# Kernel optimization log

Hardware: AMD Instinct MI355X
Metric: run time of the kernel (lower is better)

## Reference

```python
import jax, jax.numpy as jnp
import numpy as np

B, H, L, E, M = 16, 8, 4096, 64, 64


def setup_inputs() -> dict:
    key = jax.random.key(0)
    k1, k2, k3 = jax.random.split(key, 3)
    x = jax.random.normal(k1, (B, H, L, E), dtype=jnp.float32)
    # nn.Parameter(torch.randn(E, E, M, 2) / sqrt(E))
    weights = jax.random.normal(k2, (E, E, M, 2), dtype=jnp.float32) / np.float32(np.sqrt(E))
    # torch.randperm(L//2)[:M].sort()[0] -> sorted unique mode indices in [0, L//2)
    index = jnp.sort(jax.random.permutation(k3, L // 2)[:M]).astype(jnp.int32)
    return {"x": x, "weights": weights, "index": index}


def reference(x, weights, index):
    Bx, Hx, Lx, Ex = x.shape
    xt = jnp.swapaxes(x, -1, -2)                      # [B,H,E,L]
    x_ft = jnp.fft.rfft(xt, axis=-1)                  # [B,H,E,L//2+1] complex64
    w_c = jax.lax.complex(weights[..., 0], weights[..., 1])  # [E,E,M] complex
    sel = x_ft[..., index]                            # gather K modes: [B,H,E,M]
    out_sel = jnp.einsum('bhei,eoi->bhoi', sel, w_c)  # per-mode complex matmul
    out_ft = jnp.zeros_like(x_ft).at[..., index].set(out_sel)  # scatter back
    out = jnp.fft.irfft(out_ft, n=Lx, axis=-1)        # [B,H,E,L] real
    return jnp.swapaxes(out, -1, -2)                  # [B,H,L,E]
```

## Files before the change

### kernel.cpp

```cpp
#include <hip/hip_runtime.h>

using half8 = __attribute__((ext_vector_type(8))) _Float16;
using f32x4 = __attribute__((ext_vector_type(4))) float;
using u16x4 = __attribute__((ext_vector_type(4))) unsigned short;

#define Lc 4096
#define Ec 64
#define Mc 64
#define BHc 128

#define TWO_PI_OVER_L 1.5339807878856412e-3f

__global__ __launch_bounds__(256) void twid_k(const int* __restrict__ idx,
                                              _Float16* __restrict__ Tt,
                                              _Float16* __restrict__ UL) {
    int id = blockIdx.x * 256 + threadIdx.x;
    {
        int l = id >> 7, m2 = id & 127, m = m2 & 63;
        int k = idx[m];
        int ph = (k * l) & (Lc - 1);
        float ang = (float)ph * TWO_PI_OVER_L;
        UL[id] = (_Float16)((m2 >= 64) ? __sinf(ang) : __cosf(ang));
    }
    {
        int m2 = id >> 12, l = id & 4095, m = m2 & 63;
        int k = idx[m];
        int ph = (k * l) & (Lc - 1);
        float ang = (float)ph * TWO_PI_OVER_L;
        Tt[id] = (_Float16)((m2 >= 64) ? -__sinf(ang) : __cosf(ang));
    }
}

#define LOADT(SET, S) do{                                                     \
    const float* g0_ = xp + (size_t)((S) * 64 + 2 * lp) * Ec;                 \
    const float* g1_ = xp + (size_t)((S) * 64 + 2 * lp + 32) * Ec;            \
    ra[SET][0] = *(const float4*)g0_;  rb[SET][0] = *(const float4*)(g0_ + Ec);\
    ra[SET][1] = *(const float4*)g1_;  rb[SET][1] = *(const float4*)(g1_ + Ec);\
}while(0)

#define PACKT(SET, BUF) do{                                                   \
    _Pragma("unroll")                                                         \
    for (int i_ = 0; i_ < 2; ++i_) {                                          \
        const float* pa_ = (const float*)&ra[SET][i_];                        \
        const float* pb_ = (const float*)&rb[SET][i_];                        \
        unsigned int pk_[4];                                                  \
        _Pragma("unroll")                                                     \
        for (int j_ = 0; j_ < 4; ++j_) {                                      \
            unsigned short ua_ = __builtin_bit_cast(unsigned short, (_Float16)pa_[j_]); \
            unsigned short ub_ = __builtin_bit_cast(unsigned short, (_Float16)pb_[j_]); \
            pk_[j_] = ua_ | ((unsigned int)ub_ << 16);                        \
        }                                                                     \
        _Pragma("unroll")                                                     \
        for (int j_ = 0; j_ < 4; ++j_) {                                      \
            int jr_ = (j_ + col4) & 3;                                        \
            int e_  = col4 * 4 + jr_;                                         \
            int byt_ = (e_ * 128 + lp * 4 + i_ * 64) ^ ((e_ & 7) << 4);       \
            *(unsigned int*)((char*)xs[BUF] + byt_) = pk_[jr_];               \
        }                                                                     \
    }                                                                         \
}while(0)

#define MFMA_STEP(S, BUF) do{                                                 \
    _Pragma("unroll")                                                         \
    for (int ks_ = 0; ks_ < 2; ++ks_) {                                       \
        half8 A0_ = *(const half8*)(tp + (S) * 64 + ks_ * 32);                \
        half8 A1_ = *(const half8*)(tp + (size_t)16 * Lc + (S) * 64 + ks_ * 32); \
        _Pragma("unroll")                                                     \
        for (int j_ = 0; j_ < 4; ++j_) {                                      \
            int rbyt_ = ((16 * j_ + lo16) * 128 + ks_ * 64 + kg * 16) ^ ((lo16 & 7) << 4); \
            half8 Bv_ = *(const half8*)((const char*)xs[BUF] + rbyt_);        \
            acc[0][j_] = __builtin_amdgcn_mfma_f32_16x16x32_f16(A0_, Bv_, acc[0][j_], 0, 0, 0); \
            acc[1][j_] = __builtin_amdgcn_mfma_f32_16x16x32_f16(A1_, Bv_, acc[1][j_], 0, 0, 0); \
        }                                                                     \
    }                                                                         \
}while(0)

template<int NCH>
__global__ __launch_bounds__(256) void fwd_k(const float* __restrict__ x,
                                             const _Float16* __restrict__ Tt,
                                             _Float16* __restrict__ selP) {
    constexpr int CH = Lc / NCH;
    constexpr int NT = CH / 64;
    __shared__ _Float16 xs[2][64 * 64];
    int bh = blockIdx.x, ch = blockIdx.y;
    int tid = threadIdx.x;
    int lane = tid & 63, w = tid >> 6;
    int lo16 = lane & 15, kg = lane >> 4;
    int col4 = tid & 15, lp = tid >> 4;

    const float* xp = x + ((size_t)bh * Lc + (size_t)ch * CH) * Ec + col4 * 4;
    const _Float16* tp = Tt + (size_t)(w * 32 + lo16) * Lc + ch * CH + kg * 8;

    float4 ra[2][2], rb[2][2];
    LOADT(0, 0);
    LOADT(1, 1);
    PACKT(0, 0);
    __syncthreads();

    f32x4 acc[2][4] = {};
    for (int t = 0; t < NT / 2; ++t) {
        int s0 = 2 * t, s1 = 2 * t + 1;
        if (s0 + 2 < NT) LOADT(0, s0 + 2);
        PACKT(1, 1);
        MFMA_STEP(s0, 0);
        __syncthreads();
        if (s1 + 2 < NT) LOADT(1, s1 + 2);
        if (s1 + 1 < NT) PACKT(0, 0);
        MFMA_STEP(s1, 1);
        __syncthreads();
    }

    _Float16* op = selP + (size_t)(ch * BHc + bh) * (128 * Ec);
    #pragma unroll
    for (int a = 0; a < 2; ++a)
        #pragma unroll
        for (int j = 0; j < 4; ++j)
            #pragma unroll
            for (int r = 0; r < 4; ++r) {
                int m2 = w * 32 + a * 16 + kg * 4 + r;
                int e  = 16 * j + lo16;
                op[m2 * Ec + e] = (_Float16)acc[a][j][r];
            }
}

__global__ __launch_bounds__(512) void mix_k(const _Float16* __restrict__ selP,
                                             const float* __restrict__ wgt,
                                             const int* __restrict__ idx,
                                             _Float16* __restrict__ Vt, int nch) {
    __shared__ float sel_s[64 * 65];
    int bh = blockIdx.x, mh = blockIdx.y;
    int tid = threadIdx.x;
    #pragma unroll
    for (int i = 0; i < 2; ++i) {
        int f4 = i * 512 + tid;
        int lr = f4 >> 4, e4 = (f4 & 15) * 4;
        int m2 = (lr < 32) ? (mh * 32 + lr) : (64 + mh * 32 + (lr - 32));
        float ax = 0.f, ay = 0.f, az = 0.f, aw = 0.f;
        for (int chn = 0; chn < nch; ++chn) {
            u16x4 v = *(const u16x4*)(selP + (size_t)(chn * BHc + bh) * 8192
                                           + (size_t)m2 * Ec + e4);
            ax += (float)__builtin_bit_cast(_Float16, (unsigned short)v[0]);
            ay += (float)__builtin_bit_cast(_Float16, (unsigned short)v[1]);
            az += (float)__builtin_bit_cast(_Float16, (unsigned short)v[2]);
            aw += (float)__builtin_bit_cast(_Float16, (unsigned short)v[3]);
        }
        float* dst = &sel_s[lr * 65 + e4];
        dst[0] = ax; dst[1] = ay; dst[2] = az; dst[3] = aw;
    }
    __syncthreads();
    int og = tid & 31, mg = tid >> 5;
    int o0 = og * 2;
    int m0 = mh * 32 + mg * 2;
    int lm = mg * 2;
    float rR[2][2] = {{0}}, rI[2][2] = {{0}};
    #pragma unroll 8
    for (int e = 0; e < Ec; ++e) {
        float sr0 = sel_s[lm * 65 + e];
        float sr1 = sel_s[(lm + 1) * 65 + e];
        float si0 = sel_s[(32 + lm) * 65 + e];
        float si1 = sel_s[(32 + lm + 1) * 65 + e];
        #pragma unroll
        for (int i = 0; i < 2; ++i) {
            const float4* wp = (const float4*)&wgt[(((size_t)e * Ec + (o0 + i)) * Mc + m0) * 2];
            float4 wv = *wp;
            rR[i][0] += sr0 * wv.x - si0 * wv.y;
            rI[i][0] += sr0 * wv.y + si0 * wv.x;
            rR[i][1] += sr1 * wv.z - si1 * wv.w;
            rI[i][1] += sr1 * wv.w + si1 * wv.z;
        }
    }
    float s0 = (idx[m0] == 0 ? 1.0f : 2.0f) / (float)Lc;
    float s1 = (idx[m0 + 1] == 0 ? 1.0f : 2.0f) / (float)Lc;
    #pragma unroll
    for (int i = 0; i < 2; ++i) {
        _Float16* vp = Vt + ((size_t)bh * 64 + o0 + i) * 128;
        unsigned short r0 = __builtin_bit_cast(unsigned short, (_Float16)(rR[i][0] * s0));
        unsigned short r1 = __builtin_bit_cast(unsigned short, (_Float16)(rR[i][1] * s1));
        unsigned short i0 = __builtin_bit_cast(unsigned short, (_Float16)(-rI[i][0] * s0));
        unsigned short i1 = __builtin_bit_cast(unsigned short, (_Float16)(-rI[i][1] * s1));
        *(unsigned int*)&vp[m0]      = r0 | ((unsigned int)r1 << 16);
        *(unsigned int*)&vp[64 + m0] = i0 | ((unsigned int)i1 << 16);
    }
}

__global__ __launch_bounds__(256) void inv_k(const _Float16* __restrict__ UL,
                                             const _Float16* __restrict__ Vt,
                                             float* __restrict__ out) {
    __shared__ _Float16 vs[64 * 136];
    int bh = blockIdx.x, lb = blockIdx.y;
    int tid = threadIdx.x, lane = tid & 63, w = tid >> 6;
    int lo16 = lane & 15, kg = lane >> 4;
    #pragma unroll
    for (int i = 0; i < 4; ++i) {
        int f = i * 256 + tid;
        int row = f >> 4, seg = f & 15;
        uint4 t4 = *(const uint4*)(Vt + (size_t)bh * 8192 + row * 128 + seg * 8);
        *(uint4*)&vs[row * 136 + seg * 8] = t4;
    }
    __syncthreads();
    int lt0 = lb * 256 + w * 64;
    const _Float16* up = UL + (size_t)(lt0 + lo16) * 128 + kg * 8;
    f32x4 acc[4][4] = {};
    #pragma unroll
    for (int ks = 0; ks < 4; ++ks) {
        half8 Af[4];
        #pragma unroll
        for (int a = 0; a < 4; ++a)
            Af[a] = *(const half8*)(up + (size_t)a * 16 * 128 + ks * 32);
        #pragma unroll
        for (int j = 0; j < 4; ++j) {
            half8 Bf = *(const half8*)&vs[(16 * j + lo16) * 136 + ks * 32 + kg * 8];
            #pragma unroll
            for (int a = 0; a < 4; ++a)
                acc[a][j] = __builtin_amdgcn_mfma_f32_16x16x32_f16(Af[a], Bf, acc[a][j], 0, 0, 0);
        }
    }
    float* op = out + ((size_t)bh * Lc + lt0) * Ec;
    #pragma unroll
    for (int a = 0; a < 4; ++a)
        #pragma unroll
        for (int j = 0; j < 4; ++j)
            #pragma unroll
            for (int r = 0; r < 4; ++r) {
                int ll = a * 16 + kg * 4 + r;
                int o  = 16 * j + lo16;
                op[ll * Ec + o] = acc[a][j][r];
            }
}

extern "C" void kernel_launch(void* const* d_in, const int* in_sizes, int n_in,
                              void* d_out, int out_size, void* d_ws, size_t ws_size,
                              hipStream_t stream) {
    const float* x   = (const float*)d_in[0];
    const float* wgt = (const float*)d_in[1];
    const int*   idx = (const int*)d_in[2];
    float* out = (float*)d_out;

    size_t tail  = (2ull * 128 * Lc + (size_t)BHc * 8192) * 2;
    size_t need8 = (size_t)8 * BHc * 8192 * 2 + tail;
    int nch = (ws_size >= need8) ? 8 : 4;

    char* ws = (char*)d_ws;
    _Float16* selP = (_Float16*)ws;
    _Float16* Tt   = (_Float16*)(ws + (size_t)nch * BHc * 8192 * 2);
    _Float16* UL   = Tt + (size_t)128 * Lc;
    _Float16* Vt   = UL + (size_t)Lc * 128;

    twid_k<<<2048, 256, 0, stream>>>(idx, Tt, UL);
    if (nch == 8)
        fwd_k<8><<<dim3(BHc, 8), 256, 0, stream>>>(x, Tt, selP);
    else
        fwd_k<4><<<dim3(BHc, 4), 256, 0, stream>>>(x, Tt, selP);
    mix_k<<<dim3(BHc, 2), 512, 0, stream>>>(selP, wgt, idx, Vt, nch);
    inv_k<<<dim3(BHc, 16), 256, 0, stream>>>(UL, Vt, out);
}
```

Measured before the change: 115.4 us.

## Compute forward twiddles in-register and fold UL generation into forward kernel

Removes the separate twiddle kernel. The forward DFT now computes its cos/sin twiddle fragments on the fly with __sinf instead of loading a precomputed fp16 table. The inverse twiddle table UL is written by the forward kernel blocks in a grid-stride loop, so one launch and the Tt table traffic disappear. In exchange, the MFMA inner loop carries 16 transcendental evaluations per k-step, which may compete with the matrix work. The UL writes also add work at the start of every forward block.

```diff
diff --git a/kernel.cpp b/kernel.cpp
--- a/kernel.cpp
+++ b/kernel.cpp
@@ -10,26 +10,8 @@
 #define BHc 128
 
 #define TWO_PI_OVER_L 1.5339807878856412e-3f
-
-__global__ __launch_bounds__(256) void twid_k(const int* __restrict__ idx,
-                                              _Float16* __restrict__ Tt,
-                                              _Float16* __restrict__ UL) {
-    int id = blockIdx.x * 256 + threadIdx.x;
-    {
-        int l = id >> 7, m2 = id & 127, m = m2 & 63;
-        int k = idx[m];
-        int ph = (k * l) & (Lc - 1);
-        float ang = (float)ph * TWO_PI_OVER_L;
-        UL[id] = (_Float16)((m2 >= 64) ? __sinf(ang) : __cosf(ang));
-    }
-    {
-        int m2 = id >> 12, l = id & 4095, m = m2 & 63;
-        int k = idx[m];
-        int ph = (k * l) & (Lc - 1);
-        float ang = (float)ph * TWO_PI_OVER_L;
-        Tt[id] = (_Float16)((m2 >= 64) ? -__sinf(ang) : __cosf(ang));
-    }
-}
+#define HALF_PI 1.5707963267948966f
+
 
 #define LOADT(SET, S) do{                                                     \
     const float* g0_ = xp + (size_t)((S) * 64 + 2 * lp) * Ec;                 \
@@ -63,8 +45,17 @@
 #define MFMA_STEP(S, BUF) do{                                                 \
     _Pragma("unroll")                                                         \
     for (int ks_ = 0; ks_ < 2; ++ks_) {                                       \
-        half8 A0_ = *(const half8*)(tp + (S) * 64 + ks_ * 32);                \
-        half8 A1_ = *(const half8*)(tp + (size_t)16 * Lc + (S) * 64 + ks_ * 32); \
+        int lb0_ = chbase + (S) * 64 + ks_ * 32 + kg * 8;                     \
+        half8 A0_, A1_;                                                       \
+        _Pragma("unroll")                                                     \
+        for (int i_ = 0; i_ < 8; ++i_) {                                      \
+            int pha_ = (ka * (lb0_ + i_)) & (Lc - 1);                         \
+            int phb_ = (kb * (lb0_ + i_)) & (Lc - 1);                         \
+            float va_ = ssgn * __sinf((float)pha_ * TWO_PI_OVER_L + soff);    \
+            float vb_ = ssgn * __sinf((float)phb_ * TWO_PI_OVER_L + soff);    \
+            A0_[i_] = (_Float16)va_;                                          \
+            A1_[i_] = (_Float16)vb_;                                          \
+        }                                                                     \
         _Pragma("unroll")                                                     \
         for (int j_ = 0; j_ < 4; ++j_) {                                      \
             int rbyt_ = ((16 * j_ + lo16) * 128 + ks_ * 64 + kg * 16) ^ ((lo16 & 7) << 4); \
@@ -77,7 +68,8 @@
 
 template<int NCH>
 __global__ __launch_bounds__(256) void fwd_k(const float* __restrict__ x,
-                                             const _Float16* __restrict__ Tt,
+                                             const int* __restrict__ idx,
+                                             _Float16* __restrict__ UL,
                                              _Float16* __restrict__ selP) {
     constexpr int CH = Lc / NCH;
     constexpr int NT = CH / 64;
@@ -88,8 +80,27 @@
     int lo16 = lane & 15, kg = lane >> 4;
     int col4 = tid & 15, lp = tid >> 4;
 
+    {
+        int bidlin = blockIdx.y * gridDim.x + blockIdx.x;
+        int stride = gridDim.x * gridDim.y * 256;
+        for (int u = bidlin * 256 + tid; u < Lc * 128; u += stride) {
+            int l_ = u >> 7, m2_ = u & 127, m_ = m2_ & 63;
+            int k_ = idx[m_];
+            int ph_ = (k_ * l_) & (Lc - 1);
+            float ang_ = (float)ph_ * TWO_PI_OVER_L;
+            UL[u] = (_Float16)((m2_ >= 64) ? __sinf(ang_) : __cosf(ang_));
+        }
+    }
+
+    int m2a = w * 32 + lo16;
+    int ka = idx[m2a & 63];
+    int kb = idx[(m2a + 16) & 63];
+    bool neg = (w >= 2);
+    float ssgn = neg ? -1.0f : 1.0f;
+    float soff = neg ? 0.0f : HALF_PI;
+    int chbase = ch * CH;
+
     const float* xp = x + ((size_t)bh * Lc + (size_t)ch * CH) * Ec + col4 * 4;
-    const _Float16* tp = Tt + (size_t)(w * 32 + lo16) * Lc + ch * CH + kg * 8;
 
     float4 ra[2][2], rb[2][2];
     LOADT(0, 0);
@@ -224,7 +235,7 @@
             for (int r = 0; r < 4; ++r) {
                 int ll = a * 16 + kg * 4 + r;
                 int o  = 16 * j + lo16;
-                op[ll * Ec + o] = acc[a][j][r];
+                op[(size_t)ll * Ec + o] = acc[a][j][r];
             }
 }
 
@@ -236,21 +247,19 @@
     const int*   idx = (const int*)d_in[2];
     float* out = (float*)d_out;
 
-    size_t tail  = (2ull * 128 * Lc + (size_t)BHc * 8192) * 2;
+    size_t tail  = ((size_t)Lc * 128 + (size_t)BHc * 8192) * 2;
     size_t need8 = (size_t)8 * BHc * 8192 * 2 + tail;
     int nch = (ws_size >= need8) ? 8 : 4;
 
     char* ws = (char*)d_ws;
     _Float16* selP = (_Float16*)ws;
-    _Float16* Tt   = (_Float16*)(ws + (size_t)nch * BHc * 8192 * 2);
-    _Float16* UL   = Tt + (size_t)128 * Lc;
+    _Float16* UL   = (_Float16*)(ws + (size_t)nch * BHc * 8192 * 2);
     _Float16* Vt   = UL + (size_t)Lc * 128;
 
-    twid_k<<<2048, 256, 0, stream>>>(idx, Tt, UL);
     if (nch == 8)
-        fwd_k<8><<<dim3(BHc, 8), 256, 0, stream>>>(x, Tt, selP);
+        fwd_k<8><<<dim3(BHc, 8), 256, 0, stream>>>(x, idx, UL, selP);
     else
-        fwd_k<4><<<dim3(BHc, 4), 256, 0, stream>>>(x, Tt, selP);
+        fwd_k<4><<<dim3(BHc, 4), 256, 0, stream>>>(x, idx, UL, selP);
     mix_k<<<dim3(BHc, 2), 512, 0, stream>>>(selP, wgt, idx, Vt, nch);
     inv_k<<<dim3(BHc, 16), 256, 0, stream>>>(UL, Vt, out);
 }
```

Result: faster. 110.7 us (median of 2 runs) (-4.1%).
